# Optimization experiments

Measured on AMD Instinct MI355X. Metric: run time of the kernel, lower is better.

## Reference

```python
import jax, jax.numpy as jnp
import numpy as np

N_NODES = 100000
NEG_SLOPE = 0.2  # PyG GATConv default


def gat_conv(x, src, dst, W, a_src, a_dst, n_nodes):
    """One PyG-style GATConv (with self-loops already appended to src/dst).
    x: [N, Fin], W: [Fin, H*C], a_src/a_dst: [H, C]. Returns [N, H, C]."""
    H, C = a_src.shape
    h = (x @ W).reshape(-1, H, C)                      # [N, H, C]
    s_src = jnp.einsum('nhc,hc->nh', h, a_src)         # [N, H]
    s_dst = jnp.einsum('nhc,hc->nh', h, a_dst)         # [N, H]
    e = jax.nn.leaky_relu(s_src[src] + s_dst[dst], NEG_SLOPE)  # [E, H]
    # segment softmax over incoming edges of each destination node
    e_max = jax.ops.segment_max(e, dst, num_segments=n_nodes)  # [N, H]
    e_exp = jnp.exp(e - e_max[dst])
    denom = jax.ops.segment_sum(e_exp, dst, num_segments=n_nodes)
    alpha = e_exp / (denom[dst] + 1e-16)               # [E, H]
    msg = h[src] * alpha[:, :, None]                   # [E, H, C]
    return jax.ops.segment_sum(msg, dst, num_segments=n_nodes)  # [N, H, C]


def setup_inputs() -> dict:
    key = jax.random.key(0)
    ks = jax.random.split(key, 10)
    in_dim, hidden, heads, out_dim = 128, 32, 4, 32
    N, E = N_NODES, 1600000
    x = jax.random.normal(ks[0], (N, in_dim), dtype=jnp.float32)
    edge_index = jax.random.randint(ks[1], (2, E), 0, N, dtype=jnp.int64)
    s = 0.1
    return {
        'x': x,
        'edge_index': edge_index,
        'W1': s * jax.random.normal(ks[2], (in_dim, heads * hidden), dtype=jnp.float32),
        'a_src1': s * jax.random.normal(ks[3], (heads, hidden), dtype=jnp.float32),
        'a_dst1': s * jax.random.normal(ks[4], (heads, hidden), dtype=jnp.float32),
        'b1': jnp.zeros((heads * hidden,), dtype=jnp.float32),
        'W2': s * jax.random.normal(ks[5], (heads * hidden, out_dim), dtype=jnp.float32),
        'a_src2': s * jax.random.normal(ks[6], (1, out_dim), dtype=jnp.float32),
        'a_dst2': s * jax.random.normal(ks[7], (1, out_dim), dtype=jnp.float32),
        'b2': jnp.zeros((out_dim,), dtype=jnp.float32),
    }


def reference(x, edge_index, W1, a_src1, a_dst1, b1, W2, a_src2, a_dst2, b2):
    N = x.shape[0]
    loops = jnp.arange(N, dtype=edge_index.dtype)
    src = jnp.concatenate([edge_index[0], loops])  # PyG adds self-loops
    dst = jnp.concatenate([edge_index[1], loops])
    h1 = gat_conv(x, src, dst, W1, a_src1, a_dst1, N)      # [N, H, C]
    h1 = jax.nn.elu(h1.reshape(N, -1) + b1)                # concat heads + bias, elu
    h2 = gat_conv(h1, src, dst, W2, a_src2, a_dst2, N)     # [N, 1, out]
    return h2.mean(axis=1) + b2                            # concat=False -> mean over heads
```

## Files before the change

### kernel.cpp

```cpp
#include <hip/hip_runtime.h>
#include <hip/hip_bf16.h>

#define NEG 0.2f
#define BK_SHIFT 9
#define BK_CAP 9216

typedef short short8 __attribute__((ext_vector_type(8)));
typedef float f32x4 __attribute__((ext_vector_type(4)));

__device__ __forceinline__ float lrelu(float x){ return x > 0.f ? x : NEG * x; }
__device__ __forceinline__ float elu_f(float x){ return x > 0.f ? x : expm1f(x); }
__device__ __forceinline__ unsigned short f2bf(float f){
  unsigned int u = __float_as_uint(f);
  unsigned int r = u + 0x7fffu + ((u >> 16) & 1u);
  return (unsigned short)(r >> 16);
}
__device__ __forceinline__ float bf2f(unsigned short u){
  return __uint_as_float(((unsigned int)u) << 16);
}
__device__ __forceinline__ float2 bfu2(unsigned int v){
  float2 r;
  r.x = __uint_as_float(v << 16);
  r.y = __uint_as_float(v & 0xffff0000u);
  return r;
}

__global__ __launch_bounds__(512) void k_binA(
    const int* __restrict__ src, const int* __restrict__ dst, int E,
    int* __restrict__ gcursor, int2* __restrict__ ebuf){
  __shared__ int hist[256];
  __shared__ int base[256];
  int t = threadIdx.x;
  if (t < 256) hist[t] = 0;
  __syncthreads();
  int e0 = blockIdx.x * 4096;
  for (int j = 0; j < 8; j++){
    int e = e0 + j * 512 + t;
    if (e < E) atomicAdd(&hist[dst[e] >> BK_SHIFT], 1);
  }
  __syncthreads();
  if (t < 256){
    int cnt = hist[t];
    if (cnt > 0) base[t] = atomicAdd(&gcursor[t], cnt);
    hist[t] = 0;
  }
  __syncthreads();
  for (int j = 0; j < 8; j++){
    int e = e0 + j * 512 + t;
    if (e < E){
      int d = dst[e]; int b = d >> BK_SHIFT;
      int loc = atomicAdd(&hist[b], 1);
      ebuf[(size_t)b * BK_CAP + base[b] + loc] = make_int2(src[e], d);
    }
  }
}

__global__ __launch_bounds__(1024) void k_csrC(
    const int2* __restrict__ ebuf, const int* __restrict__ gcount,
    int* __restrict__ rowp, int* __restrict__ csr, int N, int NBK, int total){
  __shared__ int hist[512];
  __shared__ int psum[256];
  __shared__ int bsum[256];
  int b = blockIdx.x, t = threadIdx.x;
  int nbase = b << BK_SHIFT;
  int cnt = gcount[b];
  const int2* eb = ebuf + (size_t)b * BK_CAP;
  if (t < 512) hist[t] = 0;
  int bv = 0;
  if (t < 256){
    int nodes = 0;
    if (t < NBK){ int nb = N - (t << BK_SHIFT); nodes = nb > 512 ? 512 : nb; bv = gcount[t] + nodes; }
    bsum[t] = bv;
  }
  __syncthreads();
  for (int off = 1; off < 256; off <<= 1){
    int x = (t >= off && t < 256) ? bsum[t - off] : 0;
    __syncthreads();
    if (t < 256) bsum[t] += x;
    __syncthreads();
  }
  for (int i = t; i < cnt; i += 1024)
    atomicAdd(&hist[eb[i].y - nbase], 1);
  __syncthreads();
  int v0 = 0, v1 = 0, ps = 0;
  if (t < 256){ v0 = hist[2 * t]; v1 = hist[2 * t + 1]; ps = v0 + v1; psum[t] = ps; }
  __syncthreads();
  for (int off = 1; off < 256; off <<= 1){
    int x = (t >= off && t < 256) ? psum[t - off] : 0;
    __syncthreads();
    if (t < 256) psum[t] += x;
    __syncthreads();
  }
  if (t < 256){
    int eo = psum[t] - ps;
    int bb = (b == 0) ? 0 : bsum[b - 1];
    int n0 = 2 * t, n1 = 2 * t + 1;
    int r0 = bb + eo + n0;
    int r1 = bb + eo + v0 + n1;
    if (nbase + n0 < N) rowp[nbase + n0] = r0;
    if (nbase + n1 < N) rowp[nbase + n1] = r1;
    hist[n0] = r0; hist[n1] = r1;
  }
  if (b == 0 && t == 0) rowp[N] = total;
  __syncthreads();
  for (int i = t; i < cnt; i += 1024){
    int2 e = eb[i];
    int pos = atomicAdd(&hist[e.y - nbase], 1);
    csr[pos] = e.x;
  }
  __syncthreads();
  if (t < 256){
    int n0 = 2 * t, n1 = 2 * t + 1;
    if (nbase + n0 < N) csr[hist[n0]] = nbase + n0;
    if (nbase + n1 < N) csr[hist[n1]] = nbase + n1;
  }
}

__global__ __launch_bounds__(128) void k_packW(
    const float* __restrict__ W, unsigned short* __restrict__ Wp){
  int n = blockIdx.x, k = threadIdx.x;
  Wp[n * 128 + k] = f2bf(W[(size_t)k * 128 + n]);
}

__global__ __launch_bounds__(256, 3) void k_gemm1(
    const float* __restrict__ x, const unsigned short* __restrict__ Wp,
    const float* __restrict__ a_src, const float* __restrict__ a_dst,
    unsigned short* __restrict__ h_bf, float* __restrict__ ss, float* __restrict__ sd, int N){
  __shared__ unsigned short Wt[128 * 136];
  __shared__ unsigned short Xb[64 * 136];
  int t = threadIdx.x;
  int rb = blockIdx.x * 64;

  #pragma unroll
  for (int j = 0; j < 8; j++){
    int fi = j * 256 + t;
    int n = fi >> 4, ch = fi & 15;
    *(uint4*)&Wt[n * 136 + ch * 8] = *(const uint4*)&Wp[n * 128 + ch * 8];
  }
  #pragma unroll
  for (int j = 0; j < 8; j++){
    int fi = j * 256 + t;
    int row = fi >> 5, k4 = (fi & 31) * 4;
    int gr = rb + row;
    float4 v = make_float4(0.f, 0.f, 0.f, 0.f);
    if (gr < N) v = *(const float4*)&x[(size_t)gr * 128 + k4];
    uint2 pk;
    pk.x = ((unsigned)f2bf(v.y) << 16) | f2bf(v.x);
    pk.y = ((unsigned)f2bf(v.w) << 16) | f2bf(v.z);
    *(uint2*)&Xb[row * 136 + k4] = pk;
  }
  __syncthreads();

  int w = t >> 6, l = t & 63;
  int m = l & 15, quad = l >> 4;
  f32x4 acc[8];
  #pragma unroll
  for (int ct = 0; ct < 8; ct++) acc[ct] = (f32x4){0.f, 0.f, 0.f, 0.f};

  #pragma unroll
  for (int kc = 0; kc < 4; kc++){
    short8 a = *(const short8*)&Xb[(w * 16 + m) * 136 + kc * 32 + quad * 8];
    #pragma unroll
    for (int ct = 0; ct < 8; ct++){
      short8 b = *(const short8*)&Wt[(ct * 16 + m) * 136 + kc * 32 + quad * 8];
      acc[ct] = __builtin_amdgcn_mfma_f32_16x16x32_bf16(a, b, acc[ct], 0, 0, 0);
    }
  }

  float as[8], ad[8];
  #pragma unroll
  for (int ct = 0; ct < 8; ct++){ as[ct] = a_src[ct * 16 + m]; ad[ct] = a_dst[ct * 16 + m]; }

  #pragma unroll
  for (int reg = 0; reg < 4; reg++){
    int gr = rb + w * 16 + quad * 4 + reg;
    bool ok = gr < N;
    if (ok){
      #pragma unroll
      for (int ct = 0; ct < 8; ct++)
        h_bf[(size_t)gr * 128 + ct * 16 + m] = f2bf(acc[ct][reg]);
    }
    #pragma unroll
    for (int hh = 0; hh < 4; hh++){
      float ps = acc[2*hh][reg] * as[2*hh] + acc[2*hh+1][reg] * as[2*hh+1];
      float pd = acc[2*hh][reg] * ad[2*hh] + acc[2*hh+1][reg] * ad[2*hh+1];
      ps += __shfl_xor(ps, 1, 16); ps += __shfl_xor(ps, 2, 16);
      ps += __shfl_xor(ps, 4, 16); ps += __shfl_xor(ps, 8, 16);
      pd += __shfl_xor(pd, 1, 16); pd += __shfl_xor(pd, 2, 16);
      pd += __shfl_xor(pd, 4, 16); pd += __shfl_xor(pd, 8, 16);
      if (m == 0 && ok){ ss[(size_t)gr * 4 + hh] = ps; sd[(size_t)gr * 4 + hh] = pd; }
    }
  }
}

__global__ __launch_bounds__(256) void k_agg1(
    const int* __restrict__ row_ptr, const int* __restrict__ csr_src,
    const float* __restrict__ ss, const float* __restrict__ sdst,
    const unsigned short* __restrict__ hb,
    unsigned int* __restrict__ out1_bf, int N){
  int n = blockIdx.x * 4 + (threadIdx.x >> 6);
  if (n >= N) return;
  int l = threadIdx.x & 63;
  int q  = (l & 7) + ((l >> 5) << 3);
  int hh = (l >> 3) & 3;
  int slot = l >> 4;
  int c = l & 15;
  int hd = c >> 2;
  float sdw = sdst[(size_t)n * 4 + hh];
  int beg = row_ptr[n], end = row_ptr[n + 1];

  float acc[8] = {0.f,0.f,0.f,0.f,0.f,0.f,0.f,0.f};
  float swacc = 0.f;

  int e = beg;
  int remaining = end - beg;
  int qc = q < remaining ? q : 0;
  int sj = csr_src[e + qc];
  float sv = ss[(size_t)sj * 4 + hh];

  while (remaining > 0){
    int cur = remaining > 16 ? 16 : remaining;
    float wv = (q < cur) ? __expf(lrelu(sv + sdw)) : 0.f;
    swacc += wv;
    int sjc = sj;
    int rn = remaining - 16;
    if (rn > 0){
      int qn = q < rn ? q : 0;
      sj = csr_src[e + 16 + qn];
      sv = ss[(size_t)sj * 4 + hh];
    }
    #pragma unroll
    for (int p = 0; p < 4; p++){
      if ((p << 2) < cur){
        int sl = ((p & 1) << 2) + slot + ((p >> 1) << 5);
        int s  = __shfl(sjc, sl, 64);
        float w = __shfl(wv, sl + (hd << 3), 64);
        uint4 u = *(const uint4*)&hb[(size_t)s * 128 + (c << 3)];
        float2 f0 = bfu2(u.x), f1 = bfu2(u.y), f2 = bfu2(u.z), f3 = bfu2(u.w);
        acc[0] += w * f0.x; acc[1] += w * f0.y;
        acc[2] += w * f1.x; acc[3] += w * f1.y;
        acc[4] += w * f2.x; acc[5] += w * f2.y;
        acc[6] += w * f3.x; acc[7] += w * f3.y;
      }
    }
    e += 16; remaining = rn;
  }

  #pragma unroll
  for (int i = 0; i < 8; i++){
    acc[i] += __shfl_xor(acc[i], 16, 64);
    acc[i] += __shfl_xor(acc[i], 32, 64);
  }
  swacc += __shfl_xor(swacc, 1, 64);
  swacc += __shfl_xor(swacc, 2, 64);
  swacc += __shfl_xor(swacc, 4, 64);
  swacc += __shfl_xor(swacc, 32, 64);
  float sw = __shfl(swacc, hd << 3, 64);
  float inv = 1.f / (sw + 1e-16f);
  if (slot == 0){
    unsigned int o0 = ((unsigned)f2bf(acc[1] * inv) << 16) | f2bf(acc[0] * inv);
    unsigned int o1 = ((unsigned)f2bf(acc[3] * inv) << 16) | f2bf(acc[2] * inv);
    unsigned int o2 = ((unsigned)f2bf(acc[5] * inv) << 16) | f2bf(acc[4] * inv);
    unsigned int o3 = ((unsigned)f2bf(acc[7] * inv) << 16) | f2bf(acc[6] * inv);
    uint4 o; o.x = o0; o.y = o1; o.z = o2; o.w = o3;
    *(uint4*)&out1_bf[(size_t)n * 64 + (c << 2)] = o;
  }
}

__global__ __launch_bounds__(256) void k_gemm2(
    const unsigned int* __restrict__ out1_bf, const float* __restrict__ b1,
    const float* __restrict__ W2,
    const float* __restrict__ a_src, const float* __restrict__ a_dst,
    unsigned short* __restrict__ h2_bf, float* __restrict__ s_src2, float* __restrict__ s_dst2, int N){
  __shared__ __align__(16) float Wl[128 * 32];
  __shared__ __align__(16) float Xl[64 * 132];
  int t = threadIdx.x;
  int rb = blockIdx.x * 64;

  const float4* Wg4 = (const float4*)W2;
  float4* Wl4 = (float4*)Wl;
  #pragma unroll
  for (int j = 0; j < 4; j++) Wl4[j * 256 + t] = Wg4[j * 256 + t];

  #pragma unroll
  for (int j = 0; j < 4; j++){
    int fi = j * 256 + t;
    int row = fi >> 4, q = fi & 15;
    int gr = rb + row;
    float v[8] = {0.f,0.f,0.f,0.f,0.f,0.f,0.f,0.f};
    if (gr < N){
      uint4 u = *(const uint4*)&out1_bf[(size_t)gr * 64 + q * 4];
      float4 bva = *(const float4*)&b1[q * 8];
      float4 bvb = *(const float4*)&b1[q * 8 + 4];
      v[0] = elu_f(bf2f((unsigned short)(u.x & 0xffff)) + bva.x);
      v[1] = elu_f(bf2f((unsigned short)(u.x >> 16))    + bva.y);
      v[2] = elu_f(bf2f((unsigned short)(u.y & 0xffff)) + bva.z);
      v[3] = elu_f(bf2f((unsigned short)(u.y >> 16))    + bva.w);
      v[4] = elu_f(bf2f((unsigned short)(u.z & 0xffff)) + bvb.x);
      v[5] = elu_f(bf2f((unsigned short)(u.z >> 16))    + bvb.y);
      v[6] = elu_f(bf2f((unsigned short)(u.w & 0xffff)) + bvb.z);
      v[7] = elu_f(bf2f((unsigned short)(u.w >> 16))    + bvb.w);
    }
    #pragma unroll
    for (int i = 0; i < 8; i++) Xl[row * 132 + q * 8 + i] = v[i];
  }
  __syncthreads();

  int cg = t & 7, rg = t >> 3;
  int c0 = cg * 4, r0 = rg * 2;
  float acc[2][4] = {};

  #pragma unroll 8
  for (int k = 0; k < 128; k++){
    float a0 = Xl[r0 * 132 + k];
    float a1 = Xl[(r0 + 1) * 132 + k];
    float4 b = *(float4*)&Wl[k * 32 + c0];
    acc[0][0] += a0 * b.x; acc[0][1] += a0 * b.y; acc[0][2] += a0 * b.z; acc[0][3] += a0 * b.w;
    acc[1][0] += a1 * b.x; acc[1][1] += a1 * b.y; acc[1][2] += a1 * b.z; acc[1][3] += a1 * b.w;
  }

  float as[4], ad[4];
  #pragma unroll
  for (int j = 0; j < 4; j++){ as[j] = a_src[c0 + j]; ad[j] = a_dst[c0 + j]; }
  #pragma unroll
  for (int i = 0; i < 2; i++){
    int row = rb + r0 + i;
    if (row < N){
      ushort4 o;
      o.x = f2bf(acc[i][0]); o.y = f2bf(acc[i][1]); o.z = f2bf(acc[i][2]); o.w = f2bf(acc[i][3]);
      *(ushort4*)&h2_bf[(size_t)row * 32 + c0] = o;
    }
    float ps = 0.f, pd = 0.f;
    #pragma unroll
    for (int j = 0; j < 4; j++){ ps += acc[i][j] * as[j]; pd += acc[i][j] * ad[j]; }
    ps += __shfl_xor(ps, 1, 8); ps += __shfl_xor(ps, 2, 8); ps += __shfl_xor(ps, 4, 8);
    pd += __shfl_xor(pd, 1, 8); pd += __shfl_xor(pd, 2, 8); pd += __shfl_xor(pd, 4, 8);
    if ((t & 7) == 0 && row < N){ s_src2[row] = ps; s_dst2[row] = pd; }
  }
}

__global__ __launch_bounds__(256) void k_agg2(
    const int* __restrict__ row_ptr, const int* __restrict__ csr_src,
    const float* __restrict__ ss2, const float* __restrict__ sd2,
    const unsigned short* __restrict__ h2bf, const float* __restrict__ b2,
    float* __restrict__ out, int N){
  int n = blockIdx.x * 4 + (threadIdx.x >> 6);
  if (n >= N) return;
  int l = threadIdx.x & 63;
  int q = l & 15;
  int slot = l >> 3;
  int ch4 = l & 7;
  float sdv = sd2[n];
  int beg = row_ptr[n], end = row_ptr[n + 1];

  float acc[4] = {0.f,0.f,0.f,0.f};
  float swacc = 0.f;

  int e = beg;
  int remaining = end - beg;
  int qc = q < remaining ? q : 0;
  int sj = csr_src[e + qc];
  float sv = ss2[sj];

  while (remaining > 0){
    int cur = remaining > 16 ? 16 : remaining;
    float wv = (q < cur) ? __expf(lrelu(sv + sdv)) : 0.f;
    swacc += wv;
    int sjc = sj;
    int rn = remaining - 16;
    if (rn > 0){
      int qn = q < rn ? q : 0;
      sj = csr_src[e + 16 + qn];
      sv = ss2[sj];
    }
    #pragma unroll
    for (int p = 0; p < 2; p++){
      if ((p << 3) < cur){
        int sl = (p << 3) + slot;
        int s  = __shfl(sjc, sl, 64);
        float w = __shfl(wv, sl, 64);
        uint2 u = *(const uint2*)&h2bf[(size_t)s * 32 + (ch4 << 2)];
        float2 f0 = bfu2(u.x), f1 = bfu2(u.y);
        acc[0] += w * f0.x; acc[1] += w * f0.y;
        acc[2] += w * f1.x; acc[3] += w * f1.y;
      }
    }
    e += 16; remaining = rn;
  }

  #pragma unroll
  for (int i = 0; i < 4; i++){
    acc[i] += __shfl_xor(acc[i], 8, 64);
    acc[i] += __shfl_xor(acc[i], 16, 64);
    acc[i] += __shfl_xor(acc[i], 32, 64);
  }
  swacc += __shfl_xor(swacc, 1, 64);
  swacc += __shfl_xor(swacc, 2, 64);
  swacc += __shfl_xor(swacc, 4, 64);
  swacc += __shfl_xor(swacc, 8, 64);
  float inv = 1.f / (swacc + 1e-16f);
  if (slot == 0){
    float4 bv = *(const float4*)&b2[ch4 << 2];
    float4 o;
    o.x = acc[0] * inv + bv.x; o.y = acc[1] * inv + bv.y;
    o.z = acc[2] * inv + bv.z; o.w = acc[3] * inv + bv.w;
    *(float4*)&out[(size_t)n * 32 + (ch4 << 2)] = o;
  }
}

extern "C" void kernel_launch(void* const* d_in, const int* in_sizes, int n_in,
                              void* d_out, int out_size, void* d_ws, size_t ws_size,
                              hipStream_t stream) {
  const float* x      = (const float*)d_in[0];
  const int*   ei     = (const int*)  d_in[1];
  const float* W1     = (const float*)d_in[2];
  const float* a_src1 = (const float*)d_in[3];
  const float* a_dst1 = (const float*)d_in[4];
  const float* b1     = (const float*)d_in[5];
  const float* W2     = (const float*)d_in[6];
  const float* a_src2 = (const float*)d_in[7];
  const float* a_dst2 = (const float*)d_in[8];
  const float* b2     = (const float*)d_in[9];
  float* out = (float*)d_out;

  int N = in_sizes[0] / 128;
  int E = in_sizes[1] / 2;
  const int* srcp = ei;
  const int* dstp = ei + E;
  int total = E + N;
  int NBK = (N + 511) >> 9;

  char* p = (char*)d_ws;
  auto alloc = [&](size_t bytes) -> void* {
    void* r = (void*)p; p += (bytes + 255) & ~(size_t)255; return r;
  };
  unsigned short* h_bf    = (unsigned short*)alloc((size_t)N * 128 * 2);
  unsigned int*   out1_bf = (unsigned int*)alloc((size_t)N * 64 * 4);
  unsigned short* h2_bf   = (unsigned short*)alloc((size_t)N * 32 * 2);
  unsigned short* Wp      = (unsigned short*)alloc(128 * 128 * 2);
  float* ss1  = (float*)alloc((size_t)N * 4 * 4);
  float* sd1  = (float*)alloc((size_t)N * 4 * 4);
  float* ss2  = (float*)alloc((size_t)N * 4);
  float* sd2  = (float*)alloc((size_t)N * 4);
  int* rowp   = (int*)alloc((size_t)(N + 1) * 4);
  int* csr    = (int*)alloc((size_t)total * 4);
  int* gcur   = (int*)alloc(256 * 4);
  int2* ebuf  = (int2*)out1_bf;
  (void)ws_size; (void)n_in; (void)out_size;

  hipMemsetAsync(gcur, 0, 256 * 4, stream);
  k_binA<<<(E + 4095) / 4096, 512, 0, stream>>>(srcp, dstp, E, gcur, ebuf);
  k_csrC<<<NBK, 1024, 0, stream>>>(ebuf, gcur, rowp, csr, N, NBK, total);

  k_packW<<<128, 128, 0, stream>>>(W1, Wp);
  k_gemm1<<<(N + 63) / 64, 256, 0, stream>>>(x, Wp, a_src1, a_dst1, h_bf, ss1, sd1, N);
  k_agg1<<<(N + 3) / 4, 256, 0, stream>>>(rowp, csr, ss1, sd1, h_bf, out1_bf, N);
  k_gemm2<<<(N + 63) / 64, 256, 0, stream>>>(out1_bf, b1, W2, a_src2, a_dst2, h2_bf, ss2, sd2, N);
  k_agg2<<<(N + 3) / 4, 256, 0, stream>>>(rowp, csr, ss2, sd2, h2_bf, b2, out, N);
}
```

Measured before the change: 313.9 us.

## Slice layer-1 features into 16-column planes and aggregate per slice

GEMM1 now writes h in eight column-sliced planes of 16 bf16 values per node, and stores s_src head-major. The layer-1 aggregation launches 8x more blocks, one per (node group, slice), so each slice's gather working set (N*32 bytes) is small enough to stay cache-resident while blocks for that slice run. It also processes 32 edges per iteration and uses nontemporal loads/stores for CSR and output. The trade-off is that each slice recomputes the edge softmax weights, issues smaller 8-byte gathers and does more shuffle reductions. GEMM2's input indexing is updated to match the sliced output layout.

```diff
diff --git a/kernel.cpp b/kernel.cpp
--- a/kernel.cpp
+++ b/kernel.cpp
@@ -125,7 +125,7 @@
 __global__ __launch_bounds__(256, 3) void k_gemm1(
     const float* __restrict__ x, const unsigned short* __restrict__ Wp,
     const float* __restrict__ a_src, const float* __restrict__ a_dst,
-    unsigned short* __restrict__ h_bf, float* __restrict__ ss, float* __restrict__ sd, int N){
+    unsigned short* __restrict__ hs, float* __restrict__ ssp, float* __restrict__ sd, int N){
   __shared__ unsigned short Wt[128 * 136];
   __shared__ unsigned short Xb[64 * 136];
   int t = threadIdx.x;
@@ -178,7 +178,7 @@
     if (ok){
       #pragma unroll
       for (int ct = 0; ct < 8; ct++)
-        h_bf[(size_t)gr * 128 + ct * 16 + m] = f2bf(acc[ct][reg]);
+        hs[(size_t)ct * N * 16 + (size_t)gr * 16 + m] = f2bf(acc[ct][reg]);
     }
     #pragma unroll
     for (int hh = 0; hh < 4; hh++){
@@ -188,87 +188,96 @@
       ps += __shfl_xor(ps, 4, 16); ps += __shfl_xor(ps, 8, 16);
       pd += __shfl_xor(pd, 1, 16); pd += __shfl_xor(pd, 2, 16);
       pd += __shfl_xor(pd, 4, 16); pd += __shfl_xor(pd, 8, 16);
-      if (m == 0 && ok){ ss[(size_t)gr * 4 + hh] = ps; sd[(size_t)gr * 4 + hh] = pd; }
-    }
-  }
-}
-
-__global__ __launch_bounds__(256) void k_agg1(
+      if (m == 0 && ok){ ssp[(size_t)hh * N + gr] = ps; sd[(size_t)gr * 4 + hh] = pd; }
+    }
+  }
+}
+
+__global__ __launch_bounds__(256) void k_agg1s(
     const int* __restrict__ row_ptr, const int* __restrict__ csr_src,
-    const float* __restrict__ ss, const float* __restrict__ sdst,
-    const unsigned short* __restrict__ hb,
-    unsigned int* __restrict__ out1_bf, int N){
-  int n = blockIdx.x * 4 + (threadIdx.x >> 6);
+    const float* __restrict__ ssp,
+    const float* __restrict__ sdst,
+    const unsigned short* __restrict__ hs,
+    unsigned int* __restrict__ out1u,
+    int N){
+  int bid = blockIdx.x;
+  int slice = bid & 7;
+  int n = (bid >> 3) * 4 + (threadIdx.x >> 6);
   if (n >= N) return;
   int l = threadIdx.x & 63;
-  int q  = (l & 7) + ((l >> 5) << 3);
-  int hh = (l >> 3) & 3;
-  int slot = l >> 4;
-  int c = l & 15;
-  int hd = c >> 2;
-  float sdw = sdst[(size_t)n * 4 + hh];
+  int q = l & 31;
+  int slot = l >> 2;
+  int ch = l & 3;
+  int head = slice >> 1;
+  const float* ssh = ssp + (size_t)head * N;
+  const unsigned short* hsl = hs + (size_t)slice * N * 16;
+  float sdw = sdst[(size_t)n * 4 + head];
   int beg = row_ptr[n], end = row_ptr[n + 1];
 
-  float acc[8] = {0.f,0.f,0.f,0.f,0.f,0.f,0.f,0.f};
-  float swacc = 0.f;
+  float acc0 = 0.f, acc1 = 0.f, acc2 = 0.f, acc3 = 0.f, swacc = 0.f;
 
   int e = beg;
   int remaining = end - beg;
   int qc = q < remaining ? q : 0;
-  int sj = csr_src[e + qc];
-  float sv = ss[(size_t)sj * 4 + hh];
+  int sj = __builtin_nontemporal_load(&csr_src[e + qc]);
+  float sv = ssh[sj];
 
   while (remaining > 0){
-    int cur = remaining > 16 ? 16 : remaining;
+    int cur = remaining > 32 ? 32 : remaining;
     float wv = (q < cur) ? __expf(lrelu(sv + sdw)) : 0.f;
     swacc += wv;
-    int sjc = sj;
-    int rn = remaining - 16;
+    int sjc = sj; float wvc = wv;
+    int rn = remaining - 32;
     if (rn > 0){
       int qn = q < rn ? q : 0;
-      sj = csr_src[e + 16 + qn];
-      sv = ss[(size_t)sj * 4 + hh];
-    }
-    #pragma unroll
-    for (int p = 0; p < 4; p++){
-      if ((p << 2) < cur){
-        int sl = ((p & 1) << 2) + slot + ((p >> 1) << 5);
-        int s  = __shfl(sjc, sl, 64);
-        float w = __shfl(wv, sl + (hd << 3), 64);
-        uint4 u = *(const uint4*)&hb[(size_t)s * 128 + (c << 3)];
-        float2 f0 = bfu2(u.x), f1 = bfu2(u.y), f2 = bfu2(u.z), f3 = bfu2(u.w);
-        acc[0] += w * f0.x; acc[1] += w * f0.y;
-        acc[2] += w * f1.x; acc[3] += w * f1.y;
-        acc[4] += w * f2.x; acc[5] += w * f2.y;
-        acc[6] += w * f3.x; acc[7] += w * f3.y;
-      }
-    }
-    e += 16; remaining = rn;
-  }
-
-  #pragma unroll
-  for (int i = 0; i < 8; i++){
-    acc[i] += __shfl_xor(acc[i], 16, 64);
-    acc[i] += __shfl_xor(acc[i], 32, 64);
-  }
+      sj = __builtin_nontemporal_load(&csr_src[e + 32 + qn]);
+      sv = ssh[sj];
+    }
+    {
+      int s  = __shfl(sjc, slot, 64);
+      float w = __shfl(wvc, slot, 64);
+      uint2 u = *(const uint2*)&hsl[(size_t)s * 16 + (ch << 2)];
+      float2 f0 = bfu2(u.x), f1 = bfu2(u.y);
+      acc0 += w * f0.x; acc1 += w * f0.y;
+      acc2 += w * f1.x; acc3 += w * f1.y;
+    }
+    if (cur > 16){
+      int s  = __shfl(sjc, 16 + slot, 64);
+      float w = __shfl(wvc, 16 + slot, 64);
+      uint2 u = *(const uint2*)&hsl[(size_t)s * 16 + (ch << 2)];
+      float2 f0 = bfu2(u.x), f1 = bfu2(u.y);
+      acc0 += w * f0.x; acc1 += w * f0.y;
+      acc2 += w * f1.x; acc3 += w * f1.y;
+    }
+    e += 32; remaining = rn;
+  }
+
   swacc += __shfl_xor(swacc, 1, 64);
   swacc += __shfl_xor(swacc, 2, 64);
   swacc += __shfl_xor(swacc, 4, 64);
-  swacc += __shfl_xor(swacc, 32, 64);
-  float sw = __shfl(swacc, hd << 3, 64);
-  float inv = 1.f / (sw + 1e-16f);
+  swacc += __shfl_xor(swacc, 8, 64);
+  swacc += __shfl_xor(swacc, 16, 64);
+  acc0 += __shfl_xor(acc0, 4, 64);  acc0 += __shfl_xor(acc0, 8, 64);
+  acc0 += __shfl_xor(acc0, 16, 64); acc0 += __shfl_xor(acc0, 32, 64);
+  acc1 += __shfl_xor(acc1, 4, 64);  acc1 += __shfl_xor(acc1, 8, 64);
+  acc1 += __shfl_xor(acc1, 16, 64); acc1 += __shfl_xor(acc1, 32, 64);
+  acc2 += __shfl_xor(acc2, 4, 64);  acc2 += __shfl_xor(acc2, 8, 64);
+  acc2 += __shfl_xor(acc2, 16, 64); acc2 += __shfl_xor(acc2, 32, 64);
+  acc3 += __shfl_xor(acc3, 4, 64);  acc3 += __shfl_xor(acc3, 8, 64);
+  acc3 += __shfl_xor(acc3, 16, 64); acc3 += __shfl_xor(acc3, 32, 64);
+
+  float inv = 1.f / (swacc + 1e-16f);
   if (slot == 0){
-    unsigned int o0 = ((unsigned)f2bf(acc[1] * inv) << 16) | f2bf(acc[0] * inv);
-    unsigned int o1 = ((unsigned)f2bf(acc[3] * inv) << 16) | f2bf(acc[2] * inv);
-    unsigned int o2 = ((unsigned)f2bf(acc[5] * inv) << 16) | f2bf(acc[4] * inv);
-    unsigned int o3 = ((unsigned)f2bf(acc[7] * inv) << 16) | f2bf(acc[6] * inv);
-    uint4 o; o.x = o0; o.y = o1; o.z = o2; o.w = o3;
-    *(uint4*)&out1_bf[(size_t)n * 64 + (c << 2)] = o;
+    unsigned int o0 = ((unsigned)f2bf(acc1 * inv) << 16) | f2bf(acc0 * inv);
+    unsigned int o1 = ((unsigned)f2bf(acc3 * inv) << 16) | f2bf(acc2 * inv);
+    unsigned long long ov = ((unsigned long long)o1 << 32) | o0;
+    __builtin_nontemporal_store(ov,
+        (unsigned long long*)&out1u[(size_t)slice * N * 8 + (size_t)n * 8 + (ch << 1)]);
   }
 }
 
 __global__ __launch_bounds__(256) void k_gemm2(
-    const unsigned int* __restrict__ out1_bf, const float* __restrict__ b1,
+    const unsigned int* __restrict__ out1u, const float* __restrict__ b1,
     const float* __restrict__ W2,
     const float* __restrict__ a_src, const float* __restrict__ a_dst,
     unsigned short* __restrict__ h2_bf, float* __restrict__ s_src2, float* __restrict__ s_dst2, int N){
@@ -289,7 +298,7 @@
     int gr = rb + row;
     float v[8] = {0.f,0.f,0.f,0.f,0.f,0.f,0.f,0.f};
     if (gr < N){
-      uint4 u = *(const uint4*)&out1_bf[(size_t)gr * 64 + q * 4];
+      uint4 u = *(const uint4*)&out1u[(size_t)(q >> 1) * N * 8 + (size_t)gr * 8 + (q & 1) * 4];
       float4 bva = *(const float4*)&b1[q * 8];
       float4 bvb = *(const float4*)&b1[q * 8 + 4];
       v[0] = elu_f(bf2f((unsigned short)(u.x & 0xffff)) + bva.x);
@@ -434,8 +443,8 @@
   auto alloc = [&](size_t bytes) -> void* {
     void* r = (void*)p; p += (bytes + 255) & ~(size_t)255; return r;
   };
-  unsigned short* h_bf    = (unsigned short*)alloc((size_t)N * 128 * 2);
-  unsigned int*   out1_bf = (unsigned int*)alloc((size_t)N * 64 * 4);
+  unsigned short* hs      = (unsigned short*)alloc((size_t)N * 128 * 2);
+  unsigned int*   out1u   = (unsigned int*)alloc((size_t)N * 64 * 4);
   unsigned short* h2_bf   = (unsigned short*)alloc((size_t)N * 32 * 2);
   unsigned short* Wp      = (unsigned short*)alloc(128 * 128 * 2);
   float* ss1  = (float*)alloc((size_t)N * 4 * 4);
@@ -445,7 +454,7 @@
   int* rowp   = (int*)alloc((size_t)(N + 1) * 4);
   int* csr    = (int*)alloc((size_t)total * 4);
   int* gcur   = (int*)alloc(256 * 4);
-  int2* ebuf  = (int2*)out1_bf;
+  int2* ebuf  = (int2*)out1u;
   (void)ws_size; (void)n_in; (void)out_size;
 
   hipMemsetAsync(gcur, 0, 256 * 4, stream);
@@ -453,8 +462,8 @@
   k_csrC<<<NBK, 1024, 0, stream>>>(ebuf, gcur, rowp, csr, N, NBK, total);
 
   k_packW<<<128, 128, 0, stream>>>(W1, Wp);
-  k_gemm1<<<(N + 63) / 64, 256, 0, stream>>>(x, Wp, a_src1, a_dst1, h_bf, ss1, sd1, N);
-  k_agg1<<<(N + 3) / 4, 256, 0, stream>>>(rowp, csr, ss1, sd1, h_bf, out1_bf, N);
-  k_gemm2<<<(N + 63) / 64, 256, 0, stream>>>(out1_bf, b1, W2, a_src2, a_dst2, h2_bf, ss2, sd2, N);
+  k_gemm1<<<(N + 63) / 64, 256, 0, stream>>>(x, Wp, a_src1, a_dst1, hs, ss1, sd1, N);
+  k_agg1s<<<((N + 3) / 4) * 8, 256, 0, stream>>>(rowp, csr, ss1, sd1, hs, out1u, N);
+  k_gemm2<<<(N + 63) / 64, 256, 0, stream>>>(out1u, b1, W2, a_src2, a_dst2, h2_bf, ss2, sd2, N);
   k_agg2<<<(N + 3) / 4, 256, 0, stream>>>(rowp, csr, ss2, sd2, h2_bf, b2, out, N);
 }
```

Result: slower. 529.0 us (+68.5%).

## Merge independent CSR build and GEMM1 launches, widen agg2 gather

Applied to the files above, without the earlier changes.

Folds the W1 bf16 packing into the edge-binning kernel as extra blocks, and merges the per-bucket CSR construction with GEMM1 into one launch via block-index dispatch, with the CSR part reusing GEMM shared memory and running at 256 threads instead of 1024. This removes two launches and lets the independent CSR and GEMM work overlap on the device. Layer-2 aggregation now gathers 16 edges per pass with 16-byte loads instead of two 8-edge passes, at the cost of an extra shuffle-reduce step. CSR index loads use nontemporal hints. The CSR blocks now run with fewer threads per bucket, which may lengthen their critical path.

```diff
diff --git a/kernel.cpp b/kernel.cpp
--- a/kernel.cpp
+++ b/kernel.cpp
@@ -25,15 +25,23 @@
   return r;
 }
 
-__global__ __launch_bounds__(512) void k_binA(
+__global__ __launch_bounds__(512) void k_binA_packW(
     const int* __restrict__ src, const int* __restrict__ dst, int E,
-    int* __restrict__ gcursor, int2* __restrict__ ebuf){
+    int* __restrict__ gcursor, int2* __restrict__ ebuf,
+    const float* __restrict__ W, unsigned short* __restrict__ Wp, int nA){
   __shared__ int hist[256];
   __shared__ int base[256];
   int t = threadIdx.x;
+  int bid = blockIdx.x;
+  if (bid >= nA){
+    int idx = (bid - nA) * 512 + t;
+    int n = idx >> 7, k = idx & 127;
+    Wp[n * 128 + k] = f2bf(W[(size_t)k * 128 + n]);
+    return;
+  }
   if (t < 256) hist[t] = 0;
   __syncthreads();
-  int e0 = blockIdx.x * 4096;
+  int e0 = bid * 4096;
   for (int j = 0; j < 8; j++){
     int e = e0 + j * 512 + t;
     if (e < E) atomicAdd(&hist[dst[e] >> BK_SHIFT], 1);
@@ -55,81 +63,78 @@
   }
 }
 
-__global__ __launch_bounds__(1024) void k_csrC(
+__global__ __launch_bounds__(256, 3) void k_csrC_gemm1(
     const int2* __restrict__ ebuf, const int* __restrict__ gcount,
-    int* __restrict__ rowp, int* __restrict__ csr, int N, int NBK, int total){
-  __shared__ int hist[512];
-  __shared__ int psum[256];
-  __shared__ int bsum[256];
-  int b = blockIdx.x, t = threadIdx.x;
-  int nbase = b << BK_SHIFT;
-  int cnt = gcount[b];
-  const int2* eb = ebuf + (size_t)b * BK_CAP;
-  if (t < 512) hist[t] = 0;
-  int bv = 0;
-  if (t < 256){
-    int nodes = 0;
-    if (t < NBK){ int nb = N - (t << BK_SHIFT); nodes = nb > 512 ? 512 : nb; bv = gcount[t] + nodes; }
-    bsum[t] = bv;
-  }
-  __syncthreads();
-  for (int off = 1; off < 256; off <<= 1){
-    int x = (t >= off && t < 256) ? bsum[t - off] : 0;
-    __syncthreads();
-    if (t < 256) bsum[t] += x;
-    __syncthreads();
-  }
-  for (int i = t; i < cnt; i += 1024)
-    atomicAdd(&hist[eb[i].y - nbase], 1);
-  __syncthreads();
-  int v0 = 0, v1 = 0, ps = 0;
-  if (t < 256){ v0 = hist[2 * t]; v1 = hist[2 * t + 1]; ps = v0 + v1; psum[t] = ps; }
-  __syncthreads();
-  for (int off = 1; off < 256; off <<= 1){
-    int x = (t >= off && t < 256) ? psum[t - off] : 0;
-    __syncthreads();
-    if (t < 256) psum[t] += x;
-    __syncthreads();
-  }
-  if (t < 256){
-    int eo = psum[t] - ps;
-    int bb = (b == 0) ? 0 : bsum[b - 1];
-    int n0 = 2 * t, n1 = 2 * t + 1;
-    int r0 = bb + eo + n0;
-    int r1 = bb + eo + v0 + n1;
-    if (nbase + n0 < N) rowp[nbase + n0] = r0;
-    if (nbase + n1 < N) rowp[nbase + n1] = r1;
-    hist[n0] = r0; hist[n1] = r1;
-  }
-  if (b == 0 && t == 0) rowp[N] = total;
-  __syncthreads();
-  for (int i = t; i < cnt; i += 1024){
-    int2 e = eb[i];
-    int pos = atomicAdd(&hist[e.y - nbase], 1);
-    csr[pos] = e.x;
-  }
-  __syncthreads();
-  if (t < 256){
-    int n0 = 2 * t, n1 = 2 * t + 1;
-    if (nbase + n0 < N) csr[hist[n0]] = nbase + n0;
-    if (nbase + n1 < N) csr[hist[n1]] = nbase + n1;
-  }
-}
-
-__global__ __launch_bounds__(128) void k_packW(
-    const float* __restrict__ W, unsigned short* __restrict__ Wp){
-  int n = blockIdx.x, k = threadIdx.x;
-  Wp[n * 128 + k] = f2bf(W[(size_t)k * 128 + n]);
-}
-
-__global__ __launch_bounds__(256, 3) void k_gemm1(
+    int* __restrict__ rowp, int* __restrict__ csr, int N, int NBK, int total,
     const float* __restrict__ x, const unsigned short* __restrict__ Wp,
     const float* __restrict__ a_src, const float* __restrict__ a_dst,
-    unsigned short* __restrict__ h_bf, float* __restrict__ ss, float* __restrict__ sd, int N){
-  __shared__ unsigned short Wt[128 * 136];
-  __shared__ unsigned short Xb[64 * 136];
+    unsigned short* __restrict__ h_bf, float* __restrict__ ss, float* __restrict__ sd){
+  __shared__ __align__(16) unsigned short Wt[128 * 136];
+  __shared__ __align__(16) unsigned short Xb[64 * 136];
   int t = threadIdx.x;
-  int rb = blockIdx.x * 64;
+
+  if (blockIdx.x < (unsigned)NBK){
+    int* hist = (int*)Wt;
+    int* psum = hist + 512;
+    int* bsum = psum + 256;
+    int b = blockIdx.x;
+    int nbase = b << BK_SHIFT;
+    int cnt = gcount[b];
+    const int2* eb = ebuf + (size_t)b * BK_CAP;
+    hist[t] = 0; hist[t + 256] = 0;
+    int bv = 0;
+    {
+      int nodes = 0;
+      if (t < NBK){ int nb = N - (t << BK_SHIFT); nodes = nb > 512 ? 512 : nb; bv = gcount[t] + nodes; }
+      bsum[t] = bv;
+    }
+    __syncthreads();
+    for (int off = 1; off < 256; off <<= 1){
+      int xv = (t >= off) ? bsum[t - off] : 0;
+      __syncthreads();
+      bsum[t] += xv;
+      __syncthreads();
+    }
+    for (int i = t; i < cnt; i += 256)
+      atomicAdd(&hist[eb[i].y - nbase], 1);
+    __syncthreads();
+    int v0 = hist[2 * t], v1 = hist[2 * t + 1];
+    int ps = v0 + v1;
+    psum[t] = ps;
+    __syncthreads();
+    for (int off = 1; off < 256; off <<= 1){
+      int xv = (t >= off) ? psum[t - off] : 0;
+      __syncthreads();
+      psum[t] += xv;
+      __syncthreads();
+    }
+    {
+      int eo = psum[t] - ps;
+      int bb = (b == 0) ? 0 : bsum[b - 1];
+      int n0 = 2 * t, n1 = 2 * t + 1;
+      int r0 = bb + eo + n0;
+      int r1 = bb + eo + v0 + n1;
+      if (nbase + n0 < N) rowp[nbase + n0] = r0;
+      if (nbase + n1 < N) rowp[nbase + n1] = r1;
+      hist[n0] = r0; hist[n1] = r1;
+    }
+    if (b == 0 && t == 0) rowp[N] = total;
+    __syncthreads();
+    for (int i = t; i < cnt; i += 256){
+      int2 e = eb[i];
+      int pos = atomicAdd(&hist[e.y - nbase], 1);
+      csr[pos] = e.x;
+    }
+    __syncthreads();
+    {
+      int n0 = 2 * t, n1 = 2 * t + 1;
+      if (nbase + n0 < N) csr[hist[n0]] = nbase + n0;
+      if (nbase + n1 < N) csr[hist[n1]] = nbase + n1;
+    }
+    return;
+  }
+
+  int rb = (blockIdx.x - NBK) * 64;
 
   #pragma unroll
   for (int j = 0; j < 8; j++){
@@ -162,8 +167,8 @@
     short8 a = *(const short8*)&Xb[(w * 16 + m) * 136 + kc * 32 + quad * 8];
     #pragma unroll
     for (int ct = 0; ct < 8; ct++){
-      short8 b = *(const short8*)&Wt[(ct * 16 + m) * 136 + kc * 32 + quad * 8];
-      acc[ct] = __builtin_amdgcn_mfma_f32_16x16x32_bf16(a, b, acc[ct], 0, 0, 0);
+      short8 bfr = *(const short8*)&Wt[(ct * 16 + m) * 136 + kc * 32 + quad * 8];
+      acc[ct] = __builtin_amdgcn_mfma_f32_16x16x32_bf16(a, bfr, acc[ct], 0, 0, 0);
     }
   }
 
@@ -182,13 +187,13 @@
     }
     #pragma unroll
     for (int hh = 0; hh < 4; hh++){
-      float ps = acc[2*hh][reg] * as[2*hh] + acc[2*hh+1][reg] * as[2*hh+1];
+      float pss = acc[2*hh][reg] * as[2*hh] + acc[2*hh+1][reg] * as[2*hh+1];
       float pd = acc[2*hh][reg] * ad[2*hh] + acc[2*hh+1][reg] * ad[2*hh+1];
-      ps += __shfl_xor(ps, 1, 16); ps += __shfl_xor(ps, 2, 16);
-      ps += __shfl_xor(ps, 4, 16); ps += __shfl_xor(ps, 8, 16);
+      pss += __shfl_xor(pss, 1, 16); pss += __shfl_xor(pss, 2, 16);
+      pss += __shfl_xor(pss, 4, 16); pss += __shfl_xor(pss, 8, 16);
       pd += __shfl_xor(pd, 1, 16); pd += __shfl_xor(pd, 2, 16);
       pd += __shfl_xor(pd, 4, 16); pd += __shfl_xor(pd, 8, 16);
-      if (m == 0 && ok){ ss[(size_t)gr * 4 + hh] = ps; sd[(size_t)gr * 4 + hh] = pd; }
+      if (m == 0 && ok){ ss[(size_t)gr * 4 + hh] = pss; sd[(size_t)gr * 4 + hh] = pd; }
     }
   }
 }
@@ -215,7 +220,7 @@
   int e = beg;
   int remaining = end - beg;
   int qc = q < remaining ? q : 0;
-  int sj = csr_src[e + qc];
+  int sj = __builtin_nontemporal_load(&csr_src[e + qc]);
   float sv = ss[(size_t)sj * 4 + hh];
 
   while (remaining > 0){
@@ -226,7 +231,7 @@
     int rn = remaining - 16;
     if (rn > 0){
       int qn = q < rn ? q : 0;
-      sj = csr_src[e + 16 + qn];
+      sj = __builtin_nontemporal_load(&csr_src[e + 16 + qn]);
       sv = ss[(size_t)sj * 4 + hh];
     }
     #pragma unroll
@@ -348,48 +353,47 @@
   if (n >= N) return;
   int l = threadIdx.x & 63;
   int q = l & 15;
-  int slot = l >> 3;
-  int ch4 = l & 7;
+  int slot = l >> 2;
+  int ch4 = l & 3;
   float sdv = sd2[n];
   int beg = row_ptr[n], end = row_ptr[n + 1];
 
-  float acc[4] = {0.f,0.f,0.f,0.f};
+  float acc[8] = {0.f,0.f,0.f,0.f,0.f,0.f,0.f,0.f};
   float swacc = 0.f;
 
   int e = beg;
   int remaining = end - beg;
   int qc = q < remaining ? q : 0;
-  int sj = csr_src[e + qc];
+  int sj = __builtin_nontemporal_load(&csr_src[e + qc]);
   float sv = ss2[sj];
 
   while (remaining > 0){
     int cur = remaining > 16 ? 16 : remaining;
     float wv = (q < cur) ? __expf(lrelu(sv + sdv)) : 0.f;
     swacc += wv;
-    int sjc = sj;
+    int sjc = sj; float wvc = wv;
     int rn = remaining - 16;
     if (rn > 0){
       int qn = q < rn ? q : 0;
-      sj = csr_src[e + 16 + qn];
+      sj = __builtin_nontemporal_load(&csr_src[e + 16 + qn]);
       sv = ss2[sj];
     }
-    #pragma unroll
-    for (int p = 0; p < 2; p++){
-      if ((p << 3) < cur){
-        int sl = (p << 3) + slot;
-        int s  = __shfl(sjc, sl, 64);
-        float w = __shfl(wv, sl, 64);
-        uint2 u = *(const uint2*)&h2bf[(size_t)s * 32 + (ch4 << 2)];
-        float2 f0 = bfu2(u.x), f1 = bfu2(u.y);
-        acc[0] += w * f0.x; acc[1] += w * f0.y;
-        acc[2] += w * f1.x; acc[3] += w * f1.y;
-      }
+    {
+      int s  = __shfl(sjc, slot, 64);
+      float w = __shfl(wvc, slot, 64);
+      uint4 u = *(const uint4*)&h2bf[(size_t)s * 32 + (ch4 << 3)];
+      float2 f0 = bfu2(u.x), f1 = bfu2(u.y), f2 = bfu2(u.z), f3 = bfu2(u.w);
+      acc[0] += w * f0.x; acc[1] += w * f0.y;
+      acc[2] += w * f1.x; acc[3] += w * f1.y;
+      acc[4] += w * f2.x; acc[5] += w * f2.y;
+      acc[6] += w * f3.x; acc[7] += w * f3.y;
     }
     e += 16; remaining = rn;
   }
 
   #pragma unroll
-  for (int i = 0; i < 4; i++){
+  for (int i = 0; i < 8; i++){
+    acc[i] += __shfl_xor(acc[i], 4, 64);
     acc[i] += __shfl_xor(acc[i], 8, 64);
     acc[i] += __shfl_xor(acc[i], 16, 64);
     acc[i] += __shfl_xor(acc[i], 32, 64);
@@ -400,11 +404,15 @@
   swacc += __shfl_xor(swacc, 8, 64);
   float inv = 1.f / (swacc + 1e-16f);
   if (slot == 0){
-    float4 bv = *(const float4*)&b2[ch4 << 2];
-    float4 o;
-    o.x = acc[0] * inv + bv.x; o.y = acc[1] * inv + bv.y;
-    o.z = acc[2] * inv + bv.z; o.w = acc[3] * inv + bv.w;
-    *(float4*)&out[(size_t)n * 32 + (ch4 << 2)] = o;
+    float4 bva = *(const float4*)&b2[(ch4 << 3)];
+    float4 bvb = *(const float4*)&b2[(ch4 << 3) + 4];
+    float4 oa, ob;
+    oa.x = acc[0] * inv + bva.x; oa.y = acc[1] * inv + bva.y;
+    oa.z = acc[2] * inv + bva.z; oa.w = acc[3] * inv + bva.w;
+    ob.x = acc[4] * inv + bvb.x; ob.y = acc[5] * inv + bvb.y;
+    ob.z = acc[6] * inv + bvb.z; ob.w = acc[7] * inv + bvb.w;
+    *(float4*)&out[(size_t)n * 32 + (ch4 << 3)] = oa;
+    *(float4*)&out[(size_t)n * 32 + (ch4 << 3) + 4] = ob;
   }
 }
 
@@ -448,13 +456,14 @@
   int2* ebuf  = (int2*)out1_bf;
   (void)ws_size; (void)n_in; (void)out_size;
 
+  int nA = (E + 4095) / 4096;
+  int nG = (N + 63) / 64;
+
   hipMemsetAsync(gcur, 0, 256 * 4, stream);
-  k_binA<<<(E + 4095) / 4096, 512, 0, stream>>>(srcp, dstp, E, gcur, ebuf);
-  k_csrC<<<NBK, 1024, 0, stream>>>(ebuf, gcur, rowp, csr, N, NBK, total);
-
-  k_packW<<<128, 128, 0, stream>>>(W1, Wp);
-  k_gemm1<<<(N + 63) / 64, 256, 0, stream>>>(x, Wp, a_src1, a_dst1, h_bf, ss1, sd1, N);
+  k_binA_packW<<<nA + 32, 512, 0, stream>>>(srcp, dstp, E, gcur, ebuf, W1, Wp, nA);
+  k_csrC_gemm1<<<NBK + nG, 256, 0, stream>>>(ebuf, gcur, rowp, csr, N, NBK, total,
+                                             x, Wp, a_src1, a_dst1, h_bf, ss1, sd1);
   k_agg1<<<(N + 3) / 4, 256, 0, stream>>>(rowp, csr, ss1, sd1, h_bf, out1_bf, N);
-  k_gemm2<<<(N + 63) / 64, 256, 0, stream>>>(out1_bf, b1, W2, a_src2, a_dst2, h2_bf, ss2, sd2, N);
+  k_gemm2<<<nG, 256, 0, stream>>>(out1_bf, b1, W2, a_src2, a_dst2, h2_bf, ss2, sd2, N);
   k_agg2<<<(N + 3) / 4, 256, 0, stream>>>(rowp, csr, ss2, sd2, h2_bf, b2, out, N);
 }
```

Result: no change. 313.6 us (-0.1%).
